# Performance work log

Hardware: AMD Instinct MI355X
Metric: run time of the kernel (lower is better)

Reference implementation:

```python
import jax, jax.numpy as jnp
import numpy as np

B, SQ, SKV = 4, 2048, 2048
IN_Q, IN_KV = 1024, 1024
H, D = 16, 64            # num_heads, hidden_channels (per-head dim)
OUT = 1024
ROPE_BASE = 4096.0


def _rope(x, base):
    # x: (..., items, D). Interleaved rotate-half RoPE over last dim.
    d = x.shape[-1]
    s = x.shape[-2]
    inv_freq = base ** (-jnp.arange(0, d, 2, dtype=x.dtype) / d)      # (D/2,)
    ang = jnp.arange(s, dtype=x.dtype)[:, None] * inv_freq[None, :]   # (S, D/2)
    cos = jnp.repeat(jnp.cos(ang), 2, axis=-1)                        # (S, D)
    sin = jnp.repeat(jnp.sin(ang), 2, axis=-1)
    xp = x.reshape(x.shape[:-1] + (d // 2, 2))
    x_rot = jnp.stack([-xp[..., 1], xp[..., 0]], axis=-1).reshape(x.shape)
    return x * cos + x_rot * sin


def setup_inputs() -> dict:
    key = jax.random.key(0)
    ks = jax.random.split(key, 8)
    sc = 0.02
    return {
        "q": jax.random.normal(ks[0], (B, SQ, IN_Q), jnp.float32),
        "kv": jax.random.normal(ks[1], (B, SKV, IN_KV), jnp.float32),
        # weights stored (in, out): y = x @ W + b  (equiv. to torch Linear)
        "Wq": jax.random.normal(ks[2], (IN_Q, H * D), jnp.float32) * sc,
        "bq": jnp.zeros((H * D,), jnp.float32),
        "Wkv": jax.random.normal(ks[3], (IN_KV, 2 * D), jnp.float32) * sc,
        "bkv": jnp.zeros((2 * D,), jnp.float32),
        "Wo": jax.random.normal(ks[4], (H * D, OUT), jnp.float32) * sc,
        "bo": jnp.zeros((OUT,), jnp.float32),
    }


def reference(q, kv, Wq, bq, Wkv, bkv, Wo, bo):
    # Q projection -> (B, H, SQ, D)
    qh = (q @ Wq + bq).reshape(B, SQ, H, D).transpose(0, 2, 1, 3)
    # KV projection (multi-query: single shared K/V head) -> (B, SKV, D) each
    kvp = kv @ Wkv + bkv
    k, v = kvp[..., :D], kvp[..., D:]
    # Rotary positional encoding on the item axis
    qh = _rope(qh, ROPE_BASE)
    k = _rope(k, ROPE_BASE)
    # Scaled dot-product attention with broadcast single-head K/V (MQA)
    scale = 1.0 / jnp.sqrt(jnp.asarray(D, qh.dtype))
    scores = jnp.einsum("bhqd,bkd->bhqk", qh, k) * scale   # (B,H,SQ,SKV)
    attn = jax.nn.softmax(scores, axis=-1)
    h = jnp.einsum("bhqk,bkd->bhqd", attn, v)              # (B,H,SQ,D)
    # Merge heads and output projection
    h = h.transpose(0, 2, 1, 3).reshape(B, SQ, H * D)
    return h @ Wo + bo
```

## Files before the change

kernel.cpp:

```cpp
#include <hip/hip_runtime.h>
#include <math.h>

typedef __bf16 bf16;
typedef __bf16 bf16x4 __attribute__((ext_vector_type(4)));
typedef __bf16 bf16x8 __attribute__((ext_vector_type(8)));
typedef float floatx4 __attribute__((ext_vector_type(4)));

#define MFMA16(a, b, c) __builtin_amdgcn_mfma_f32_16x16x32_bf16(a, b, c, 0, 0, 0)

#if __has_builtin(__builtin_amdgcn_exp2f)
#define EXP2F(x) __builtin_amdgcn_exp2f(x)
#else
#define EXP2F(x) exp2f(x)
#endif

constexpr int Bc = 4, SQc = 2048, SKVc = 2048, Hc = 16, Dc = 64;
#define QSCALE 0.18033688011112042f

__device__ __forceinline__ void glds16(const bf16* g, bf16* lds_base, int lane) {
#if __has_builtin(__builtin_amdgcn_global_load_lds)
  __builtin_amdgcn_global_load_lds(
      (const __attribute__((address_space(1))) void*)g,
      (__attribute__((address_space(3))) void*)lds_base, 16, 0, 0);
#else
  *(bf16x8*)(lds_base + 8 * lane) = *(const bf16x8*)g;
#endif
}

__global__ void cvt_bf16(const float* __restrict__ in, bf16* __restrict__ out) {
  const size_t i = ((size_t)blockIdx.x * 256 + threadIdx.x) * 4;
  const float4 v = *(const float4*)&in[i];
  bf16x4 o = {(bf16)v.x, (bf16)v.y, (bf16)v.z, (bf16)v.w};
  *(bf16x4*)&out[i] = o;
}

__global__ void rope_tab_build(float2* __restrict__ tab) {
  const int i = blockIdx.x * 256 + threadIdx.x;
  const int pos = i >> 5, f = i & 31;
  const float ang = (float)pos * exp2f(-0.375f * (float)f);
  float sn, cs;
  sincosf(ang, &sn, &cs);
  tab[i] = make_float2(cs, sn);
}

__global__ void transpose_cvt(const float* __restrict__ in, bf16* __restrict__ out,
                              int K, int N) {
  __shared__ bf16 T[64][72];
  const int tid = threadIdx.x;
  const int n0 = blockIdx.x * 64, k0 = blockIdx.y * 64;
  const int tr = tid >> 4, tc4 = (tid & 15) * 4;
#pragma unroll
  for (int i = 0; i < 4; i++) {
    const int k = tr + 16 * i;
    const float4 v = *(const float4*)&in[(size_t)(k0 + k) * N + n0 + tc4];
    T[tc4 + 0][k] = (bf16)v.x;
    T[tc4 + 1][k] = (bf16)v.y;
    T[tc4 + 2][k] = (bf16)v.z;
    T[tc4 + 3][k] = (bf16)v.w;
  }
  __syncthreads();
  const int nr = tid >> 2, kc = (tid & 3) * 8;
#pragma unroll
  for (int hf = 0; hf < 2; hf++)
    *(bf16x8*)&out[(size_t)(n0 + nr) * K + k0 + kc + 32 * hf] =
        *(const bf16x8*)&T[nr][kc + 32 * hf];
}

__device__ __forceinline__ void gemm_kloop(const bf16* __restrict__ A,
                                           const bf16* __restrict__ BT, int m0,
                                           int n0, int tid, int wave, int lane,
                                           int m, int g, bf16* As, bf16* Bs,
                                           floatx4 (*acc)[4], int mq, int nq) {
  const int r_ = tid >> 3, p_ = tid & 7;
  const bf16* pA[4];
  const bf16* pB[4];
#pragma unroll
  for (int q = 0; q < 4; q++) {
    const int r = r_ + q * 32;
    const int s = p_ ^ (r & 7);
    pA[q] = &A[(size_t)(m0 + r) * 1024 + 8 * s];
    pB[q] = &BT[(size_t)(n0 + r) * 1024 + 8 * s];
  }

  for (int k0 = 0; k0 < 1024; k0 += 64) {
    __syncthreads();
#pragma unroll
    for (int q = 0; q < 4; q++) {
      glds16(pA[q] + k0, &As[(q * 4 + wave) * 512], lane);
      glds16(pB[q] + k0, &Bs[(q * 4 + wave) * 512], lane);
    }
    __syncthreads();

    bf16x8 bb[4][2];
#pragma unroll
    for (int j = 0; j < 4; j++) {
      const int row = nq + 16 * j + m;
#pragma unroll
      for (int kh = 0; kh < 2; kh++)
        bb[j][kh] = *(const bf16x8*)&Bs[row * 64 + 8 * ((g + 4 * kh) ^ (row & 7))];
    }
#pragma unroll
    for (int i = 0; i < 4; i++) {
      const int row = mq + 16 * i + m;
      const bf16x8 a0 = *(const bf16x8*)&As[row * 64 + 8 * (g ^ (row & 7))];
      const bf16x8 a1 = *(const bf16x8*)&As[row * 64 + 8 * ((g + 4) ^ (row & 7))];
#pragma unroll
      for (int j = 0; j < 4; j++) {
        acc[i][j] = MFMA16(a0, bb[j][0], acc[i][j]);
        acc[i][j] = MFMA16(a1, bb[j][1], acc[i][j]);
      }
    }
  }
}

__global__ __launch_bounds__(256, 3) void gemm_qkv(
    const bf16* __restrict__ qA, const bf16* __restrict__ qBT,
    const float* __restrict__ qb, const bf16* __restrict__ kvA,
    const bf16* __restrict__ kvBT, const float* __restrict__ kvb,
    const float2* __restrict__ tab, bf16* __restrict__ qh,
    bf16* __restrict__ kko, bf16* __restrict__ vto) {
  __shared__ bf16 As[128 * 64];
  __shared__ bf16 Bs[128 * 64];

  const int tid = threadIdx.x, lane = tid & 63, wave = tid >> 6;
  const int m = lane & 15, g = lane >> 4;
  const int m0 = blockIdx.x * 128;
  const bool isQ = (blockIdx.y < 8);
  const int n0 = isQ ? blockIdx.y * 128 : 0;
  const bf16* A = isQ ? qA : kvA;
  const bf16* BT = isQ ? qBT : kvBT;
  const float* bias = isQ ? qb : kvb;
  const int mq = (wave >> 1) * 64, nq = (wave & 1) * 64;

  floatx4 z = {0.f, 0.f, 0.f, 0.f};
  floatx4 acc[4][4];
#pragma unroll
  for (int i = 0; i < 4; i++)
#pragma unroll
    for (int j = 0; j < 4; j++) acc[i][j] = z;

  gemm_kloop(A, BT, m0, n0, tid, wave, lane, m, g, As, Bs, acc, mq, nq);

  const int rq = 4 * g;
#pragma unroll
  for (int j = 0; j < 4; j++) {
    const int col = n0 + nq + 16 * j + m;
    const float bv = bias[col];
#pragma unroll
    for (int i = 0; i < 4; i++) {
#pragma unroll
      for (int r = 0; r < 4; r++) {
        const int row = m0 + mq + 16 * i + rq + r;
        float v = acc[i][j][r] + bv;
        const float vp = __shfl_xor(v, 1);
        if (isQ) {
          const int d = col & 63, hh = col >> 6;
          const int pos = row & (SQc - 1), b = row >> 11;
          const float2 cssn = tab[pos * 32 + (d >> 1)];
          const float res = (d & 1) ? (v * cssn.x + vp * cssn.y)
                                    : (v * cssn.x - vp * cssn.y);
          qh[(((size_t)(b * Hc + hh) * SQc) + pos) * Dc + d] = (bf16)(res * QSCALE);
        } else {
          const int pos = row & (SKVc - 1), b = row >> 11;
          const size_t fb = (size_t)b * (SKVc * Dc);
          if (col < 64) {
            const int d = col;
            const float2 cssn = tab[pos * 32 + (d >> 1)];
            const float res = (d & 1) ? (v * cssn.x + vp * cssn.y)
                                      : (v * cssn.x - vp * cssn.y);
            const int kc = (pos >> 4) * 2 + (d >> 5);
            const int kl = ((d >> 3) & 3) * 16 + (pos & 15);
            kko[fb + (size_t)kc * 512 + kl * 8 + (d & 7)] = (bf16)res;
          } else {
            const int d = col - 64;
            const int vc = (pos >> 6) * 8 + (d >> 4) * 2 + ((pos >> 5) & 1);
            const int vl = ((pos >> 3) & 3) * 16 + (d & 15);
            vto[fb + (size_t)vc * 512 + vl * 8 + (pos & 7)] = (bf16)v;
          }
        }
      }
    }
  }
}

__global__ __launch_bounds__(256, 3) void gemm_out(
    const bf16* __restrict__ A, const bf16* __restrict__ BT,
    const float* __restrict__ bias, float* __restrict__ out) {
  __shared__ bf16 As[128 * 64];
  __shared__ bf16 Bs[128 * 64];

  const int tid = threadIdx.x, lane = tid & 63, wave = tid >> 6;
  const int m = lane & 15, g = lane >> 4;
  const int m0 = blockIdx.x * 128, n0 = blockIdx.y * 128;
  const int mq = (wave >> 1) * 64, nq = (wave & 1) * 64;

  floatx4 z = {0.f, 0.f, 0.f, 0.f};
  floatx4 acc[4][4];
#pragma unroll
  for (int i = 0; i < 4; i++)
#pragma unroll
    for (int j = 0; j < 4; j++) acc[i][j] = z;

  gemm_kloop(A, BT, m0, n0, tid, wave, lane, m, g, As, Bs, acc, mq, nq);

  const int rq = 4 * g;
#pragma unroll
  for (int j = 0; j < 4; j++) {
    const int col = n0 + nq + 16 * j + m;
    const float bv = bias[col];
#pragma unroll
    for (int i = 0; i < 4; i++)
#pragma unroll
      for (int r = 0; r < 4; r++) {
        const int row = m0 + mq + 16 * i + rq + r;
        out[(size_t)row * 1024 + col] = acc[i][j][r] + bv;
      }
  }
}

__global__ __launch_bounds__(512, 4) void attn_v5(
    const bf16* __restrict__ qh, const bf16* __restrict__ kk,
    const bf16* __restrict__ vt, bf16* __restrict__ hout) {
  const int bid = blockIdx.x;
  const int qt = bid & 7, h = (bid >> 3) & 15, b = bid >> 7;
  const int tid = threadIdx.x, lane = tid & 63, wave = tid >> 6;
  const int m = lane & 15, g = lane >> 4;

  __shared__ bf16 Kb[2][4096];
  __shared__ bf16 Vb[4096];
  __shared__ bf16 Pb[8][2][16][68];

  const int q0 = qt * 256 + wave * 32;
  const bf16* qp = qh + (((size_t)(b * Hc + h) * SQc) + q0 + m) * Dc + 8 * g;
  bf16x8 bq[2][2];
#pragma unroll
  for (int s = 0; s < 2; s++) {
    bq[s][0] = *(const bf16x8*)(qp + (size_t)(16 * s) * Dc);
    bq[s][1] = *(const bf16x8*)(qp + (size_t)(16 * s) * Dc + 32);
  }

  const bf16 one = (bf16)1.0f;
  const bf16x8 ones = {one, one, one, one, one, one, one, one};

  floatx4 z = {0.f, 0.f, 0.f, 0.f};
  floatx4 accO[2][4];
  floatx4 lacc[2] = {z, z};
#pragma unroll
  for (int s = 0; s < 2; s++)
#pragma unroll
    for (int t = 0; t < 4; t++) accO[s][t] = z;

  const size_t fb = (size_t)b * (SKVc * Dc);
  const bf16* kg = kk + fb + 8 * lane;
  const bf16* vg = vt + fb + 8 * lane;

  glds16(kg + (size_t)wave * 512, &Kb[0][wave * 512], lane);
  __syncthreads();

  for (int it = 0; it < 32; ++it) {
    const int cur = it & 1;
    if (it) __syncthreads();
    glds16(vg + (size_t)(it * 8 + wave) * 512, &Vb[wave * 512], lane);
    if (it + 1 < 32)
      glds16(kg + (size_t)((it + 1) * 8 + wave) * 512, &Kb[cur ^ 1][wave * 512],
             lane);

    bf16x8 kfr[4][2];
#pragma unroll
    for (int c = 0; c < 4; c++) {
      kfr[c][0] = *(const bf16x8*)&Kb[cur][(2 * c + 0) * 512 + 8 * lane];
      kfr[c][1] = *(const bf16x8*)&Kb[cur][(2 * c + 1) * 512 + 8 * lane];
    }
#pragma unroll
    for (int s = 0; s < 2; s++) {
#pragma unroll
      for (int c = 0; c < 4; c++) {
        floatx4 sv = MFMA16(kfr[c][0], bq[s][0], z);
        sv = MFMA16(kfr[c][1], bq[s][1], sv);
        bf16x4 pk = {(bf16)EXP2F(sv[0]), (bf16)EXP2F(sv[1]), (bf16)EXP2F(sv[2]),
                     (bf16)EXP2F(sv[3])};
        *(bf16x4*)&Pb[wave][s][m][16 * c + 4 * g] = pk;
      }
    }
    __syncthreads();

    bf16x8 vf[4][2];
#pragma unroll
    for (int t = 0; t < 4; t++) {
      vf[t][0] = *(const bf16x8*)&Vb[(2 * t + 0) * 512 + 8 * lane];
      vf[t][1] = *(const bf16x8*)&Vb[(2 * t + 1) * 512 + 8 * lane];
    }
#pragma unroll
    for (int s = 0; s < 2; s++) {
      const bf16x8 pa0 = *(const bf16x8*)&Pb[wave][s][m][8 * g];
      const bf16x8 pa1 = *(const bf16x8*)&Pb[wave][s][m][32 + 8 * g];
      lacc[s] = MFMA16(pa0, ones, lacc[s]);
      lacc[s] = MFMA16(pa1, ones, lacc[s]);
#pragma unroll
      for (int t = 0; t < 4; t++) {
        accO[s][t] = MFMA16(pa0, vf[t][0], accO[s][t]);
        accO[s][t] = MFMA16(pa1, vf[t][1], accO[s][t]);
      }
    }
  }

#pragma unroll
  for (int s = 0; s < 2; s++) {
    floatx4 inv;
#pragma unroll
    for (int r = 0; r < 4; r++) inv[r] = 1.0f / lacc[s][r];
#pragma unroll
    for (int t = 0; t < 4; t++)
#pragma unroll
      for (int r = 0; r < 4; r++) {
        const int qrow = q0 + 16 * s + 4 * g + r;
        hout[((size_t)(b * SQc + qrow)) * (Hc * Dc) + h * Dc + 16 * t + m] =
            (bf16)(accO[s][t][r] * inv[r]);
      }
  }
}

extern "C" void kernel_launch(void* const* d_in, const int* in_sizes, int n_in,
                              void* d_out, int out_size, void* d_ws, size_t ws_size,
                              hipStream_t stream) {
  const float* q = (const float*)d_in[0];
  const float* kv = (const float*)d_in[1];
  const float* Wq = (const float*)d_in[2];
  const float* bq = (const float*)d_in[3];
  const float* Wkv = (const float*)d_in[4];
  const float* bkv = (const float*)d_in[5];
  const float* Wo = (const float*)d_in[6];
  const float* bo = (const float*)d_in[7];

  char* ws = (char*)d_ws;
  bf16* qbf = (bf16*)ws;
  bf16* kvbf = (bf16*)(ws + ((size_t)16 << 20));
  bf16* WqT = (bf16*)(ws + ((size_t)32 << 20));
  bf16* WkvT = (bf16*)(ws + ((size_t)34 << 20));
  float2* rtab = (float2*)(ws + ((size_t)34 << 20) + ((size_t)256 << 10));
  bf16* WoT = (bf16*)(ws + ((size_t)35 << 20));
  bf16* qh = (bf16*)(ws + ((size_t)37 << 20));
  bf16* kk = (bf16*)(ws + ((size_t)53 << 20));
  bf16* vt = (bf16*)(ws + ((size_t)54 << 20));
  bf16* hh = qbf;

  const int M = Bc * SQc;

  rope_tab_build<<<256, 256, 0, stream>>>(rtab);
  cvt_bf16<<<M, 256, 0, stream>>>(q, qbf);
  cvt_bf16<<<M, 256, 0, stream>>>(kv, kvbf);
  transpose_cvt<<<dim3(16, 16), 256, 0, stream>>>(Wq, WqT, 1024, 1024);
  transpose_cvt<<<dim3(2, 16), 256, 0, stream>>>(Wkv, WkvT, 1024, 128);
  transpose_cvt<<<dim3(16, 16), 256, 0, stream>>>(Wo, WoT, 1024, 1024);

  gemm_qkv<<<dim3(64, 9), 256, 0, stream>>>(qbf, WqT, bq, kvbf, WkvT, bkv, rtab,
                                            qh, kk, vt);
  attn_v5<<<Bc * Hc * (SQc / 256), 512, 0, stream>>>(qh, kk, vt, hh);
  gemm_out<<<dim3(64, 8), 256, 0, stream>>>(hh, WoT, bo, (float*)d_out);
}
```

Baseline: 261.4 us.

## Store GEMM operands in MFMA fragment order and load directly from global memory

The converters and the attention epilogue now write the activations and weights in an MFMA-fragment-tiled layout. This lets the projection GEMMs skip LDS staging and barriers and load register fragments straight from global memory, with a one-step B prefetch. Tiles become 256x64 per block with each wave owning 64 rows, so the same B fragments are read by every wave through cache rather than shared via LDS. It also raises wave priority around the PV MFMA section in attention. The risk is more global and L2 traffic from the lost LDS reuse and exposed load latency.

```diff
diff --git a/kernel.cpp b/kernel.cpp
--- a/kernel.cpp
+++ b/kernel.cpp
@@ -16,6 +16,7 @@
 
 constexpr int Bc = 4, SQc = 2048, SKVc = 2048, Hc = 16, Dc = 64;
 #define QSCALE 0.18033688011112042f
+
 
 __device__ __forceinline__ void glds16(const bf16* g, bf16* lds_base, int lane) {
 #if __has_builtin(__builtin_amdgcn_global_load_lds)
@@ -27,11 +28,15 @@
 #endif
 }
 
-__global__ void cvt_bf16(const float* __restrict__ in, bf16* __restrict__ out) {
-  const size_t i = ((size_t)blockIdx.x * 256 + threadIdx.x) * 4;
-  const float4 v = *(const float4*)&in[i];
+__global__ void cvt_bf16_frag(const float* __restrict__ in,
+                              bf16* __restrict__ out) {
+  const int row = blockIdx.x;
+  const int k = threadIdx.x * 4;
+  const float4 v = *(const float4*)&in[(size_t)row * 1024 + k];
   bf16x4 o = {(bf16)v.x, (bf16)v.y, (bf16)v.z, (bf16)v.w};
-  *(bf16x4*)&out[i] = o;
+  const size_t idx = (size_t)(row >> 4) * 16384 + (k >> 5) * 512 +
+                     ((k >> 3) & 3) * 128 + (row & 15) * 8 + (k & 7);
+  *(bf16x4*)&out[idx] = o;
 }
 
 __global__ void rope_tab_build(float2* __restrict__ tab) {
@@ -61,76 +66,72 @@
   __syncthreads();
   const int nr = tid >> 2, kc = (tid & 3) * 8;
 #pragma unroll
-  for (int hf = 0; hf < 2; hf++)
-    *(bf16x8*)&out[(size_t)(n0 + nr) * K + k0 + kc + 32 * hf] =
-        *(const bf16x8*)&T[nr][kc + 32 * hf];
-}
-
-__device__ __forceinline__ void gemm_kloop(const bf16* __restrict__ A,
-                                           const bf16* __restrict__ BT, int m0,
-                                           int n0, int tid, int wave, int lane,
-                                           int m, int g, bf16* As, bf16* Bs,
-                                           floatx4 (*acc)[4], int mq, int nq) {
-  const int r_ = tid >> 3, p_ = tid & 7;
-  const bf16* pA[4];
-  const bf16* pB[4];
-#pragma unroll
-  for (int q = 0; q < 4; q++) {
-    const int r = r_ + q * 32;
-    const int s = p_ ^ (r & 7);
-    pA[q] = &A[(size_t)(m0 + r) * 1024 + 8 * s];
-    pB[q] = &BT[(size_t)(n0 + r) * 1024 + 8 * s];
-  }
-
-  for (int k0 = 0; k0 < 1024; k0 += 64) {
-    __syncthreads();
-#pragma unroll
-    for (int q = 0; q < 4; q++) {
-      glds16(pA[q] + k0, &As[(q * 4 + wave) * 512], lane);
-      glds16(pB[q] + k0, &Bs[(q * 4 + wave) * 512], lane);
-    }
-    __syncthreads();
-
-    bf16x8 bb[4][2];
-#pragma unroll
-    for (int j = 0; j < 4; j++) {
-      const int row = nq + 16 * j + m;
-#pragma unroll
-      for (int kh = 0; kh < 2; kh++)
-        bb[j][kh] = *(const bf16x8*)&Bs[row * 64 + 8 * ((g + 4 * kh) ^ (row & 7))];
-    }
+  for (int hf = 0; hf < 2; hf++) {
+    const int n = n0 + nr, k = k0 + kc + 32 * hf;
+    const size_t idx = (size_t)((n >> 4) * (K >> 5) + (k >> 5)) * 512 +
+                       ((k >> 3) & 3) * 128 + (n & 15) * 8;
+    *(bf16x8*)&out[idx] = *(const bf16x8*)&T[nr][kc + 32 * hf];
+  }
+}
+
+__device__ __forceinline__ void gemm_fd_loop(const bf16* __restrict__ Ab,
+                                             const bf16* __restrict__ Bb,
+                                             floatx4 (*acc)[4]) {
+  bf16x8 bfr[4][2];
+#pragma unroll
+  for (int j = 0; j < 4; j++) {
+    bfr[j][0] = *(const bf16x8*)(Bb + (size_t)j * 16384);
+    bfr[j][1] = *(const bf16x8*)(Bb + (size_t)j * 16384 + 512);
+  }
+  for (int t = 0; t < 16; ++t) {
+    const size_t c = (size_t)(2 * t) * 512;
+    bf16x8 af[4][2];
 #pragma unroll
     for (int i = 0; i < 4; i++) {
-      const int row = mq + 16 * i + m;
-      const bf16x8 a0 = *(const bf16x8*)&As[row * 64 + 8 * (g ^ (row & 7))];
-      const bf16x8 a1 = *(const bf16x8*)&As[row * 64 + 8 * ((g + 4) ^ (row & 7))];
+      af[i][0] = *(const bf16x8*)(Ab + (size_t)i * 16384 + c);
+      af[i][1] = *(const bf16x8*)(Ab + (size_t)i * 16384 + c + 512);
+    }
+    bf16x8 bn[4][2];
+    if (t < 15) {
 #pragma unroll
       for (int j = 0; j < 4; j++) {
-        acc[i][j] = MFMA16(a0, bb[j][0], acc[i][j]);
-        acc[i][j] = MFMA16(a1, bb[j][1], acc[i][j]);
-      }
-    }
-  }
-}
-
-__global__ __launch_bounds__(256, 3) void gemm_qkv(
+        bn[j][0] = *(const bf16x8*)(Bb + (size_t)j * 16384 + c + 1024);
+        bn[j][1] = *(const bf16x8*)(Bb + (size_t)j * 16384 + c + 1536);
+      }
+    }
+#pragma unroll
+    for (int i = 0; i < 4; i++)
+#pragma unroll
+      for (int j = 0; j < 4; j++) {
+        acc[i][j] = MFMA16(af[i][0], bfr[j][0], acc[i][j]);
+        acc[i][j] = MFMA16(af[i][1], bfr[j][1], acc[i][j]);
+      }
+    if (t < 15) {
+#pragma unroll
+      for (int j = 0; j < 4; j++) {
+        bfr[j][0] = bn[j][0];
+        bfr[j][1] = bn[j][1];
+      }
+    }
+  }
+}
+
+__global__ __launch_bounds__(256, 2) void gemm_qkv(
     const bf16* __restrict__ qA, const bf16* __restrict__ qBT,
     const float* __restrict__ qb, const bf16* __restrict__ kvA,
     const bf16* __restrict__ kvBT, const float* __restrict__ kvb,
     const float2* __restrict__ tab, bf16* __restrict__ qh,
     bf16* __restrict__ kko, bf16* __restrict__ vto) {
-  __shared__ bf16 As[128 * 64];
-  __shared__ bf16 Bs[128 * 64];
-
   const int tid = threadIdx.x, lane = tid & 63, wave = tid >> 6;
   const int m = lane & 15, g = lane >> 4;
-  const int m0 = blockIdx.x * 128;
-  const bool isQ = (blockIdx.y < 8);
-  const int n0 = isQ ? blockIdx.y * 128 : 0;
-  const bf16* A = isQ ? qA : kvA;
-  const bf16* BT = isQ ? qBT : kvBT;
-  const float* bias = isQ ? qb : kvb;
-  const int mq = (wave >> 1) * 64, nq = (wave & 1) * 64;
+  const int m0 = blockIdx.x * 256;
+  const int mode = (blockIdx.y < 16) ? 0 : (blockIdx.y == 16 ? 1 : 2);
+  const bf16* A = (mode == 0) ? qA : kvA;
+  const bf16* BT = (mode == 0) ? qBT : kvBT;
+  const int nb = (mode == 0) ? blockIdx.y * 64 : (mode == 1 ? 0 : 64);
+
+  const bf16* Ab = A + (size_t)((m0 + wave * 64) >> 4) * 16384 + 8 * lane;
+  const bf16* Bb = BT + (size_t)(nb >> 4) * 16384 + 8 * lane;
 
   floatx4 z = {0.f, 0.f, 0.f, 0.f};
   floatx4 acc[4][4];
@@ -139,60 +140,57 @@
 #pragma unroll
     for (int j = 0; j < 4; j++) acc[i][j] = z;
 
-  gemm_kloop(A, BT, m0, n0, tid, wave, lane, m, g, As, Bs, acc, mq, nq);
+  gemm_fd_loop(Ab, Bb, acc);
 
   const int rq = 4 * g;
 #pragma unroll
   for (int j = 0; j < 4; j++) {
-    const int col = n0 + nq + 16 * j + m;
-    const float bv = bias[col];
+    const int col = nb + 16 * j + m;
+    const float bv = (mode == 0) ? qb[col] : kvb[col];
 #pragma unroll
     for (int i = 0; i < 4; i++) {
 #pragma unroll
       for (int r = 0; r < 4; r++) {
-        const int row = m0 + mq + 16 * i + rq + r;
+        const int row = m0 + wave * 64 + 16 * i + rq + r;
         float v = acc[i][j][r] + bv;
         const float vp = __shfl_xor(v, 1);
-        if (isQ) {
+        const int pos = row & (SQc - 1), b = row >> 11;
+        if (mode == 0) {
           const int d = col & 63, hh = col >> 6;
-          const int pos = row & (SQc - 1), b = row >> 11;
           const float2 cssn = tab[pos * 32 + (d >> 1)];
           const float res = (d & 1) ? (v * cssn.x + vp * cssn.y)
                                     : (v * cssn.x - vp * cssn.y);
           qh[(((size_t)(b * Hc + hh) * SQc) + pos) * Dc + d] = (bf16)(res * QSCALE);
+        } else if (mode == 1) {
+          const int d = 16 * j + m;
+          const float2 cssn = tab[pos * 32 + (d >> 1)];
+          const float res = (d & 1) ? (v * cssn.x + vp * cssn.y)
+                                    : (v * cssn.x - vp * cssn.y);
+          const size_t fb = (size_t)b * (SKVc * Dc);
+          const int kc = (pos >> 4) * 2 + (d >> 5);
+          const int kl = ((d >> 3) & 3) * 16 + (pos & 15);
+          kko[fb + (size_t)kc * 512 + kl * 8 + (d & 7)] = (bf16)res;
         } else {
-          const int pos = row & (SKVc - 1), b = row >> 11;
+          const int d = 16 * j + m;
           const size_t fb = (size_t)b * (SKVc * Dc);
-          if (col < 64) {
-            const int d = col;
-            const float2 cssn = tab[pos * 32 + (d >> 1)];
-            const float res = (d & 1) ? (v * cssn.x + vp * cssn.y)
-                                      : (v * cssn.x - vp * cssn.y);
-            const int kc = (pos >> 4) * 2 + (d >> 5);
-            const int kl = ((d >> 3) & 3) * 16 + (pos & 15);
-            kko[fb + (size_t)kc * 512 + kl * 8 + (d & 7)] = (bf16)res;
-          } else {
-            const int d = col - 64;
-            const int vc = (pos >> 6) * 8 + (d >> 4) * 2 + ((pos >> 5) & 1);
-            const int vl = ((pos >> 3) & 3) * 16 + (d & 15);
-            vto[fb + (size_t)vc * 512 + vl * 8 + (pos & 7)] = (bf16)v;
-          }
+          const int vc = (pos >> 6) * 8 + (d >> 4) * 2 + ((pos >> 5) & 1);
+          const int vl = ((pos >> 3) & 3) * 16 + (d & 15);
+          vto[fb + (size_t)vc * 512 + vl * 8 + (pos & 7)] = (bf16)v;
         }
       }
     }
   }
 }
 
-__global__ __launch_bounds__(256, 3) void gemm_out(
+__global__ __launch_bounds__(256, 2) void gemm_out(
     const bf16* __restrict__ A, const bf16* __restrict__ BT,
     const float* __restrict__ bias, float* __restrict__ out) {
-  __shared__ bf16 As[128 * 64];
-  __shared__ bf16 Bs[128 * 64];
-
   const int tid = threadIdx.x, lane = tid & 63, wave = tid >> 6;
   const int m = lane & 15, g = lane >> 4;
-  const int m0 = blockIdx.x * 128, n0 = blockIdx.y * 128;
-  const int mq = (wave >> 1) * 64, nq = (wave & 1) * 64;
+  const int m0 = blockIdx.x * 256, n0 = blockIdx.y * 64;
+
+  const bf16* Ab = A + (size_t)((m0 + wave * 64) >> 4) * 16384 + 8 * lane;
+  const bf16* Bb = BT + (size_t)(n0 >> 4) * 16384 + 8 * lane;
 
   floatx4 z = {0.f, 0.f, 0.f, 0.f};
   floatx4 acc[4][4];
@@ -201,18 +199,18 @@
 #pragma unroll
     for (int j = 0; j < 4; j++) acc[i][j] = z;
 
-  gemm_kloop(A, BT, m0, n0, tid, wave, lane, m, g, As, Bs, acc, mq, nq);
+  gemm_fd_loop(Ab, Bb, acc);
 
   const int rq = 4 * g;
 #pragma unroll
   for (int j = 0; j < 4; j++) {
-    const int col = n0 + nq + 16 * j + m;
+    const int col = n0 + 16 * j + m;
     const float bv = bias[col];
 #pragma unroll
     for (int i = 0; i < 4; i++)
 #pragma unroll
       for (int r = 0; r < 4; r++) {
-        const int row = m0 + mq + 16 * i + rq + r;
+        const int row = m0 + wave * 64 + 16 * i + rq + r;
         out[(size_t)row * 1024 + col] = acc[i][j][r] + bv;
       }
   }
@@ -290,6 +288,7 @@
       vf[t][0] = *(const bf16x8*)&Vb[(2 * t + 0) * 512 + 8 * lane];
       vf[t][1] = *(const bf16x8*)&Vb[(2 * t + 1) * 512 + 8 * lane];
     }
+    __builtin_amdgcn_s_setprio(1);
 #pragma unroll
     for (int s = 0; s < 2; s++) {
       const bf16x8 pa0 = *(const bf16x8*)&Pb[wave][s][m][8 * g];
@@ -302,6 +301,7 @@
         accO[s][t] = MFMA16(pa1, vf[t][1], accO[s][t]);
       }
     }
+    __builtin_amdgcn_s_setprio(0);
   }
 
 #pragma unroll
@@ -314,8 +314,11 @@
 #pragma unroll
       for (int r = 0; r < 4; r++) {
         const int qrow = q0 + 16 * s + 4 * g + r;
-        hout[((size_t)(b * SQc + qrow)) * (Hc * Dc) + h * Dc + 16 * t + m] =
-            (bf16)(accO[s][t][r] * inv[r]);
+        const int row = b * SQc + qrow;
+        const int col = h * 64 + 16 * t + m;
+        const size_t idx = (size_t)(row >> 4) * 16384 + (col >> 5) * 512 +
+                           ((col >> 3) & 3) * 128 + (row & 15) * 8 + (col & 7);
+        hout[idx] = (bf16)(accO[s][t][r] * inv[r]);
       }
   }
 }
@@ -347,14 +350,14 @@
   const int M = Bc * SQc;
 
   rope_tab_build<<<256, 256, 0, stream>>>(rtab);
-  cvt_bf16<<<M, 256, 0, stream>>>(q, qbf);
-  cvt_bf16<<<M, 256, 0, stream>>>(kv, kvbf);
+  cvt_bf16_frag<<<M, 256, 0, stream>>>(q, qbf);
+  cvt_bf16_frag<<<M, 256, 0, stream>>>(kv, kvbf);
   transpose_cvt<<<dim3(16, 16), 256, 0, stream>>>(Wq, WqT, 1024, 1024);
   transpose_cvt<<<dim3(2, 16), 256, 0, stream>>>(Wkv, WkvT, 1024, 128);
   transpose_cvt<<<dim3(16, 16), 256, 0, stream>>>(Wo, WoT, 1024, 1024);
 
-  gemm_qkv<<<dim3(64, 9), 256, 0, stream>>>(qbf, WqT, bq, kvbf, WkvT, bkv, rtab,
-                                            qh, kk, vt);
+  gemm_qkv<<<dim3(32, 18), 256, 0, stream>>>(qbf, WqT, bq, kvbf, WkvT, bkv, rtab,
+                                             qh, kk, vt);
   attn_v5<<<Bc * Hc * (SQc / 256), 512, 0, stream>>>(qh, kk, vt, hh);
-  gemm_out<<<dim3(64, 8), 256, 0, stream>>>(hh, WoT, bo, (float*)d_out);
-}
+  gemm_out<<<dim3(32, 16), 256, 0, stream>>>(hh, WoT, bo, (float*)d_out);
+}
```

Result: slower. 290.8 us (+11.2%).

## Switch projection GEMMs to 32x32x16 MFMA and raise attention PV priority

Applied to the files above, without the earlier changes.

Rewrites the shared GEMM inner loop and both epilogues to use 32x32x16 bf16 MFMA with 2x2 floatx16 accumulators per wave instead of 4x4 16x16x32 tiles. The goal is fewer LDS fragment loads per FLOP and higher MFMA throughput. Occupancy launch bounds drop from 3 to 2 blocks per SM. In attention, the PV MFMA section is wrapped in s_setprio to favour matrix issue across waves.

```diff
diff --git a/kernel.cpp b/kernel.cpp
--- a/kernel.cpp
+++ b/kernel.cpp
@@ -5,8 +5,10 @@
 typedef __bf16 bf16x4 __attribute__((ext_vector_type(4)));
 typedef __bf16 bf16x8 __attribute__((ext_vector_type(8)));
 typedef float floatx4 __attribute__((ext_vector_type(4)));
+typedef float floatx16 __attribute__((ext_vector_type(16)));
 
 #define MFMA16(a, b, c) __builtin_amdgcn_mfma_f32_16x16x32_bf16(a, b, c, 0, 0, 0)
+#define MFMA32(a, b, c) __builtin_amdgcn_mfma_f32_32x32x16_bf16(a, b, c, 0, 0, 0)
 
 #if __has_builtin(__builtin_amdgcn_exp2f)
 #define EXP2F(x) __builtin_amdgcn_exp2f(x)
@@ -69,8 +71,8 @@
 __device__ __forceinline__ void gemm_kloop(const bf16* __restrict__ A,
                                            const bf16* __restrict__ BT, int m0,
                                            int n0, int tid, int wave, int lane,
-                                           int m, int g, bf16* As, bf16* Bs,
-                                           floatx4 (*acc)[4], int mq, int nq) {
+                                           bf16* As, bf16* Bs,
+                                           floatx16 (*acc)[2]) {
   const int r_ = tid >> 3, p_ = tid & 7;
   const bf16* pA[4];
   const bf16* pB[4];
@@ -81,6 +83,9 @@
     pA[q] = &A[(size_t)(m0 + r) * 1024 + 8 * s];
     pB[q] = &BT[(size_t)(n0 + r) * 1024 + 8 * s];
   }
+  const int rl = lane & 31, h = lane >> 5;
+  const int ar = (wave >> 1) * 64 + rl;
+  const int br = (wave & 1) * 64 + rl;
 
   for (int k0 = 0; k0 < 1024; k0 += 64) {
     __syncthreads();
@@ -91,29 +96,30 @@
     }
     __syncthreads();
 
-    bf16x8 bb[4][2];
-#pragma unroll
-    for (int j = 0; j < 4; j++) {
-      const int row = nq + 16 * j + m;
-#pragma unroll
-      for (int kh = 0; kh < 2; kh++)
-        bb[j][kh] = *(const bf16x8*)&Bs[row * 64 + 8 * ((g + 4 * kh) ^ (row & 7))];
-    }
-#pragma unroll
-    for (int i = 0; i < 4; i++) {
-      const int row = mq + 16 * i + m;
-      const bf16x8 a0 = *(const bf16x8*)&As[row * 64 + 8 * (g ^ (row & 7))];
-      const bf16x8 a1 = *(const bf16x8*)&As[row * 64 + 8 * ((g + 4) ^ (row & 7))];
-#pragma unroll
-      for (int j = 0; j < 4; j++) {
-        acc[i][j] = MFMA16(a0, bb[j][0], acc[i][j]);
-        acc[i][j] = MFMA16(a1, bb[j][1], acc[i][j]);
-      }
-    }
-  }
-}
-
-__global__ __launch_bounds__(256, 3) void gemm_qkv(
+#pragma unroll
+    for (int s = 0; s < 4; s++) {
+      const int c = 2 * s + h;
+      bf16x8 af[2], bfr[2];
+#pragma unroll
+      for (int i = 0; i < 2; i++) {
+        const int r = ar + 32 * i;
+        af[i] = *(const bf16x8*)&As[r * 64 + 8 * (c ^ (r & 7))];
+      }
+#pragma unroll
+      for (int j = 0; j < 2; j++) {
+        const int r = br + 32 * j;
+        bfr[j] = *(const bf16x8*)&Bs[r * 64 + 8 * (c ^ (r & 7))];
+      }
+#pragma unroll
+      for (int i = 0; i < 2; i++)
+#pragma unroll
+        for (int j = 0; j < 2; j++)
+          acc[i][j] = MFMA32(af[i], bfr[j], acc[i][j]);
+    }
+  }
+}
+
+__global__ __launch_bounds__(256, 2) void gemm_qkv(
     const bf16* __restrict__ qA, const bf16* __restrict__ qBT,
     const float* __restrict__ qb, const bf16* __restrict__ kvA,
     const bf16* __restrict__ kvBT, const float* __restrict__ kvb,
@@ -123,35 +129,35 @@
   __shared__ bf16 Bs[128 * 64];
 
   const int tid = threadIdx.x, lane = tid & 63, wave = tid >> 6;
-  const int m = lane & 15, g = lane >> 4;
+  const int rl = lane & 31, h = lane >> 5;
   const int m0 = blockIdx.x * 128;
   const bool isQ = (blockIdx.y < 8);
   const int n0 = isQ ? blockIdx.y * 128 : 0;
   const bf16* A = isQ ? qA : kvA;
   const bf16* BT = isQ ? qBT : kvBT;
   const float* bias = isQ ? qb : kvb;
-  const int mq = (wave >> 1) * 64, nq = (wave & 1) * 64;
-
-  floatx4 z = {0.f, 0.f, 0.f, 0.f};
-  floatx4 acc[4][4];
-#pragma unroll
-  for (int i = 0; i < 4; i++)
-#pragma unroll
-    for (int j = 0; j < 4; j++) acc[i][j] = z;
-
-  gemm_kloop(A, BT, m0, n0, tid, wave, lane, m, g, As, Bs, acc, mq, nq);
-
-  const int rq = 4 * g;
-#pragma unroll
-  for (int j = 0; j < 4; j++) {
-    const int col = n0 + nq + 16 * j + m;
+
+  floatx16 acc[2][2];
+#pragma unroll
+  for (int i = 0; i < 2; i++)
+#pragma unroll
+    for (int j = 0; j < 2; j++)
+#pragma unroll
+      for (int t = 0; t < 16; t++) acc[i][j][t] = 0.f;
+
+  gemm_kloop(A, BT, m0, n0, tid, wave, lane, As, Bs, acc);
+
+#pragma unroll
+  for (int j = 0; j < 2; j++) {
+    const int col = n0 + (wave & 1) * 64 + 32 * j + rl;
     const float bv = bias[col];
 #pragma unroll
-    for (int i = 0; i < 4; i++) {
-#pragma unroll
-      for (int r = 0; r < 4; r++) {
-        const int row = m0 + mq + 16 * i + rq + r;
-        float v = acc[i][j][r] + bv;
+    for (int i = 0; i < 2; i++) {
+#pragma unroll
+      for (int t = 0; t < 16; t++) {
+        const int row =
+            m0 + (wave >> 1) * 64 + 32 * i + (t & 3) + 8 * (t >> 2) + 4 * h;
+        float v = acc[i][j][t] + bv;
         const float vp = __shfl_xor(v, 1);
         if (isQ) {
           const int d = col & 63, hh = col >> 6;
@@ -183,37 +189,37 @@
   }
 }
 
-__global__ __launch_bounds__(256, 3) void gemm_out(
+__global__ __launch_bounds__(256, 2) void gemm_out(
     const bf16* __restrict__ A, const bf16* __restrict__ BT,
     const float* __restrict__ bias, float* __restrict__ out) {
   __shared__ bf16 As[128 * 64];
   __shared__ bf16 Bs[128 * 64];
 
   const int tid = threadIdx.x, lane = tid & 63, wave = tid >> 6;
-  const int m = lane & 15, g = lane >> 4;
+  const int rl = lane & 31, h = lane >> 5;
   const int m0 = blockIdx.x * 128, n0 = blockIdx.y * 128;
-  const int mq = (wave >> 1) * 64, nq = (wave & 1) * 64;
-
-  floatx4 z = {0.f, 0.f, 0.f, 0.f};
-  floatx4 acc[4][4];
-#pragma unroll
-  for (int i = 0; i < 4; i++)
-#pragma unroll
-    for (int j = 0; j < 4; j++) acc[i][j] = z;
-
-  gemm_kloop(A, BT, m0, n0, tid, wave, lane, m, g, As, Bs, acc, mq, nq);
-
-  const int rq = 4 * g;
-#pragma unroll
-  for (int j = 0; j < 4; j++) {
-    const int col = n0 + nq + 16 * j + m;
+
+  floatx16 acc[2][2];
+#pragma unroll
+  for (int i = 0; i < 2; i++)
+#pragma unroll
+    for (int j = 0; j < 2; j++)
+#pragma unroll
+      for (int t = 0; t < 16; t++) acc[i][j][t] = 0.f;
+
+  gemm_kloop(A, BT, m0, n0, tid, wave, lane, As, Bs, acc);
+
+#pragma unroll
+  for (int j = 0; j < 2; j++) {
+    const int col = n0 + (wave & 1) * 64 + 32 * j + rl;
     const float bv = bias[col];
 #pragma unroll
-    for (int i = 0; i < 4; i++)
-#pragma unroll
-      for (int r = 0; r < 4; r++) {
-        const int row = m0 + mq + 16 * i + rq + r;
-        out[(size_t)row * 1024 + col] = acc[i][j][r] + bv;
+    for (int i = 0; i < 2; i++)
+#pragma unroll
+      for (int t = 0; t < 16; t++) {
+        const int row =
+            m0 + (wave >> 1) * 64 + 32 * i + (t & 3) + 8 * (t >> 2) + 4 * h;
+        out[(size_t)row * 1024 + col] = acc[i][j][t] + bv;
       }
   }
 }
@@ -290,6 +296,7 @@
       vf[t][0] = *(const bf16x8*)&Vb[(2 * t + 0) * 512 + 8 * lane];
       vf[t][1] = *(const bf16x8*)&Vb[(2 * t + 1) * 512 + 8 * lane];
     }
+    __builtin_amdgcn_s_setprio(1);
 #pragma unroll
     for (int s = 0; s < 2; s++) {
       const bf16x8 pa0 = *(const bf16x8*)&Pb[wave][s][m][8 * g];
@@ -302,6 +309,7 @@
         accO[s][t] = MFMA16(pa1, vf[t][1], accO[s][t]);
       }
     }
+    __builtin_amdgcn_s_setprio(0);
   }
 
 #pragma unroll
```

Result: no change. 266.5 us (+2.0%).
